# Kernel tuning notes

Hardware: AMD Instinct MI355X
Metric: run time of the kernel (lower is better)

The kernel has to match this reference:

```python
import jax, jax.numpy as jnp
import numpy as np

B, C, H, W = 4, 384, 248, 216
NUM_ANCHORS = 6           # len(rotations)=2 * len(sizes)=3
NUM_CLASSES = 3
BOX_CODE_SIZE = 7
CLS_OUT = NUM_ANCHORS * NUM_CLASSES      # 18
REG_OUT = NUM_ANCHORS * BOX_CODE_SIZE    # 42
DIR_OUT = NUM_ANCHORS * 2                # 12


def setup_inputs() -> dict:
    key = jax.random.key(0)
    ks = jax.random.split(key, 4)
    x = jax.random.normal(ks[0], (B, C, H, W), dtype=jnp.float32)
    scale = 0.02
    w_cls = jax.random.normal(ks[1], (C, CLS_OUT), dtype=jnp.float32) * scale
    w_reg = jax.random.normal(ks[2], (C, REG_OUT), dtype=jnp.float32) * scale
    w_dir = jax.random.normal(ks[3], (C, DIR_OUT), dtype=jnp.float32) * scale
    b_cls = jnp.zeros((CLS_OUT,), dtype=jnp.float32)
    b_reg = jnp.zeros((REG_OUT,), dtype=jnp.float32)
    b_dir = jnp.zeros((DIR_OUT,), dtype=jnp.float32)
    return {"x": x, "w_cls": w_cls, "b_cls": b_cls, "w_reg": w_reg,
            "b_reg": b_reg, "w_dir": w_dir, "b_dir": b_dir}


def _conv1x1(x, w, b):
    # channels_first 1x1 conv == per-pixel matmul over channels
    return jnp.einsum('bchw,co->bohw', x, w) + b[None, :, None, None]


def reference(x, w_cls, b_cls, w_reg, b_reg, w_dir, b_dir):
    cls_score = _conv1x1(x, w_cls, b_cls)      # [B, 18, H, W]
    bbox_pred = _conv1x1(x, w_reg, b_reg)      # [B, 42, H, W]
    dir_cls_preds = _conv1x1(x, w_dir, b_dir)  # [B, 12, H, W]
    return (cls_score, bbox_pred, dir_cls_preds)
```

## Files before the change

### kernel.cpp

```cpp
#include <hip/hip_runtime.h>


constexpr int Bn   = 4;
constexpr int Cc   = 384;
constexpr int Hh   = 248;
constexpr int Ww   = 216;
constexpr int HW   = Hh * Ww;
constexpr int NPIX = Bn * HW;
constexpr int NCLS = 18;
constexpr int NREG = 42;
constexpr int NDIR = 12;

typedef float v2f __attribute__((ext_vector_type(2)));

__global__ __launch_bounds__(256) void head_fused(
    const float* __restrict__ x,
    const float* __restrict__ wc, const float* __restrict__ bc,
    const float* __restrict__ wr, const float* __restrict__ br,
    const float* __restrict__ wd, const float* __restrict__ bd,
    float* __restrict__ out)
{
    const int g = blockIdx.x * 256 + threadIdx.x;
    const int b = g / HW;
    const int p = g - b * HW;

    const float* __restrict__ xb = x + (size_t)b * Cc * HW + p;

    v2f ac[NCLS / 2];
    v2f ar[NREG / 2];
    v2f ad[NDIR / 2];
    #pragma unroll
    for (int o = 0; o < NCLS / 2; ++o) { ac[o][0] = bc[2*o]; ac[o][1] = bc[2*o+1]; }
    #pragma unroll
    for (int o = 0; o < NREG / 2; ++o) { ar[o][0] = br[2*o]; ar[o][1] = br[2*o+1]; }
    #pragma unroll
    for (int o = 0; o < NDIR / 2; ++o) { ad[o][0] = bd[2*o]; ad[o][1] = bd[2*o+1]; }

    for (int c = 0; c < Cc; ++c) {
        const float xs = xb[(size_t)c * HW];
        v2f xv; xv[0] = xs; xv[1] = xs;

        const v2f* __restrict__ wcc = (const v2f*)(wc + c * NCLS);
        #pragma unroll
        for (int o = 0; o < NCLS / 2; ++o)
            ac[o] = __builtin_elementwise_fma(xv, wcc[o], ac[o]);

        const v2f* __restrict__ wrc = (const v2f*)(wr + c * NREG);
        #pragma unroll
        for (int o = 0; o < NREG / 2; ++o)
            ar[o] = __builtin_elementwise_fma(xv, wrc[o], ar[o]);

        const v2f* __restrict__ wdc = (const v2f*)(wd + c * NDIR);
        #pragma unroll
        for (int o = 0; o < NDIR / 2; ++o)
            ad[o] = __builtin_elementwise_fma(xv, wdc[o], ad[o]);
    }

    float* __restrict__ oc = out + (size_t)b * NCLS * HW + p;
    #pragma unroll
    for (int o = 0; o < NCLS / 2; ++o) {
        oc[(size_t)(2*o)   * HW] = ac[o][0];
        oc[(size_t)(2*o+1) * HW] = ac[o][1];
    }
    float* __restrict__ og = out + (size_t)Bn * NCLS * HW + (size_t)b * NREG * HW + p;
    #pragma unroll
    for (int o = 0; o < NREG / 2; ++o) {
        og[(size_t)(2*o)   * HW] = ar[o][0];
        og[(size_t)(2*o+1) * HW] = ar[o][1];
    }
    float* __restrict__ od = out + (size_t)Bn * (NCLS + NREG) * HW + (size_t)b * NDIR * HW + p;
    #pragma unroll
    for (int o = 0; o < NDIR / 2; ++o) {
        od[(size_t)(2*o)   * HW] = ad[o][0];
        od[(size_t)(2*o+1) * HW] = ad[o][1];
    }
}

extern "C" void kernel_launch(void* const* d_in, const int* in_sizes, int n_in,
                              void* d_out, int out_size, void* d_ws, size_t ws_size,
                              hipStream_t stream) {
    const float* x  = (const float*)d_in[0];
    const float* wc = (const float*)d_in[1];
    const float* bc = (const float*)d_in[2];
    const float* wr = (const float*)d_in[3];
    const float* br = (const float*)d_in[4];
    const float* wd = (const float*)d_in[5];
    const float* bd = (const float*)d_in[6];
    float* out = (float*)d_out;

    dim3 grid(NPIX / 256);
    dim3 block(256);
    head_fused<<<grid, block, 0, stream>>>(x, wc, bc, wr, br, wd, bd, out);
}
```

Baseline: 619.3 us.

## Split output channels across four wavefronts per 64-pixel block

```diff
diff --git a/kernel.cpp b/kernel.cpp
--- a/kernel.cpp
+++ b/kernel.cpp
@@ -11,68 +11,68 @@
 constexpr int NREG = 42;
 constexpr int NDIR = 12;
 
-typedef float v2f __attribute__((ext_vector_type(2)));
+template<int NA, int LDA, int NB, int LDB>
+__device__ __forceinline__ void cohort_run(
+    const float* __restrict__ xb,
+    const float* __restrict__ wA, const float* __restrict__ bA,
+    float* __restrict__ oA,
+    const float* __restrict__ wB, const float* __restrict__ bB,
+    float* __restrict__ oB)
+{
+    float acc[NA + NB];
+    #pragma unroll
+    for (int j = 0; j < NA; ++j) acc[j] = bA[j];
+    #pragma unroll
+    for (int j = 0; j < NB; ++j) acc[NA + j] = bB[j];
 
-__global__ __launch_bounds__(256) void head_fused(
+    #pragma unroll 4
+    for (int c = 0; c < Cc; ++c) {
+        const float xv = xb[(size_t)c * HW];
+        #pragma unroll
+        for (int j = 0; j < NA; ++j)
+            acc[j] = fmaf(xv, wA[c * LDA + j], acc[j]);
+        #pragma unroll
+        for (int j = 0; j < NB; ++j)
+            acc[NA + j] = fmaf(xv, wB[c * LDB + j], acc[NA + j]);
+    }
+
+    #pragma unroll
+    for (int j = 0; j < NA; ++j) oA[(size_t)j * HW] = acc[j];
+    #pragma unroll
+    for (int j = 0; j < NB; ++j) oB[(size_t)j * HW] = acc[NA + j];
+}
+
+__global__ __launch_bounds__(256) void head_fused_msplit(
     const float* __restrict__ x,
     const float* __restrict__ wc, const float* __restrict__ bc,
     const float* __restrict__ wr, const float* __restrict__ br,
     const float* __restrict__ wd, const float* __restrict__ bd,
     float* __restrict__ out)
 {
-    const int g = blockIdx.x * 256 + threadIdx.x;
-    const int b = g / HW;
-    const int p = g - b * HW;
+    const int w    = threadIdx.x >> 6;
+    const int lane = threadIdx.x & 63;
+    const int pix  = blockIdx.x * 64 + lane;
+    const int b    = pix / HW;
+    const int p    = pix - b * HW;
 
     const float* __restrict__ xb = x + (size_t)b * Cc * HW + p;
 
-    v2f ac[NCLS / 2];
-    v2f ar[NREG / 2];
-    v2f ad[NDIR / 2];
-    #pragma unroll
-    for (int o = 0; o < NCLS / 2; ++o) { ac[o][0] = bc[2*o]; ac[o][1] = bc[2*o+1]; }
-    #pragma unroll
-    for (int o = 0; o < NREG / 2; ++o) { ar[o][0] = br[2*o]; ar[o][1] = br[2*o+1]; }
-    #pragma unroll
-    for (int o = 0; o < NDIR / 2; ++o) { ad[o][0] = bd[2*o]; ad[o][1] = bd[2*o+1]; }
+    float* __restrict__ outc = out + (size_t)b * NCLS * HW + p;
+    float* __restrict__ outr = out + (size_t)Bn * NCLS * HW
+                                   + (size_t)b * NREG * HW + p;
+    float* __restrict__ outd = out + (size_t)Bn * (NCLS + NREG) * HW
+                                   + (size_t)b * NDIR * HW + p;
 
-    for (int c = 0; c < Cc; ++c) {
-        const float xs = xb[(size_t)c * HW];
-        v2f xv; xv[0] = xs; xv[1] = xs;
-
-        const v2f* __restrict__ wcc = (const v2f*)(wc + c * NCLS);
-        #pragma unroll
-        for (int o = 0; o < NCLS / 2; ++o)
-            ac[o] = __builtin_elementwise_fma(xv, wcc[o], ac[o]);
-
-        const v2f* __restrict__ wrc = (const v2f*)(wr + c * NREG);
-        #pragma unroll
-        for (int o = 0; o < NREG / 2; ++o)
-            ar[o] = __builtin_elementwise_fma(xv, wrc[o], ar[o]);
-
-        const v2f* __restrict__ wdc = (const v2f*)(wd + c * NDIR);
-        #pragma unroll
-        for (int o = 0; o < NDIR / 2; ++o)
-            ad[o] = __builtin_elementwise_fma(xv, wdc[o], ad[o]);
-    }
-
-    float* __restrict__ oc = out + (size_t)b * NCLS * HW + p;
-    #pragma unroll
-    for (int o = 0; o < NCLS / 2; ++o) {
-        oc[(size_t)(2*o)   * HW] = ac[o][0];
-        oc[(size_t)(2*o+1) * HW] = ac[o][1];
-    }
-    float* __restrict__ og = out + (size_t)Bn * NCLS * HW + (size_t)b * NREG * HW + p;
-    #pragma unroll
-    for (int o = 0; o < NREG / 2; ++o) {
-        og[(size_t)(2*o)   * HW] = ar[o][0];
-        og[(size_t)(2*o+1) * HW] = ar[o][1];
-    }
-    float* __restrict__ od = out + (size_t)Bn * (NCLS + NREG) * HW + (size_t)b * NDIR * HW + p;
-    #pragma unroll
-    for (int o = 0; o < NDIR / 2; ++o) {
-        od[(size_t)(2*o)   * HW] = ad[o][0];
-        od[(size_t)(2*o+1) * HW] = ad[o][1];
+    if (w == 0) {
+        cohort_run<18, NCLS, 0, 1>(xb, wc, bc, outc, wc, bc, outc);
+    } else if (w == 1) {
+        cohort_run<18, NREG, 0, 1>(xb, wr, br, outr, wr, br, outr);
+    } else if (w == 2) {
+        cohort_run<18, NREG, 0, 1>(xb, wr + 18, br + 18, outr + (size_t)18 * HW,
+                                   wr, br, outr);
+    } else {
+        cohort_run<6, NREG, 12, NDIR>(xb, wr + 36, br + 36, outr + (size_t)36 * HW,
+                                      wd, bd, outd);
     }
 }
 
@@ -88,7 +88,7 @@
     const float* bd = (const float*)d_in[6];
     float* out = (float*)d_out;
 
-    dim3 grid(NPIX / 256);
+    dim3 grid(NPIX / 64);
     dim3 block(256);
-    head_fused<<<grid, block, 0, stream>>>(x, wc, bc, wr, br, wd, bd, out);
+    head_fused_msplit<<<grid, block, 0, stream>>>(x, wc, bc, wr, br, wd, bd, out);
 }
```

New measurement: 531.5 us. -14.2%, faster.
